# Optimization experiments

Hardware: AMD Instinct MI355X
Metric: run time of the kernel (lower is better)

Reference implementation:

```python
import jax, jax.numpy as jnp
import numpy as np
from math import sqrt

SCALE = sqrt(512.0)  # max(key_size, attn_hidden_size, query_size) with scaled=True

def setup_inputs() -> dict:
    key = jax.random.key(0)
    k1, k2, k3, k4, k5 = jax.random.split(key, 5)
    B, T, S, M, N, H = 8, 512, 512, 512, 512, 128
    return {
        "query": jax.random.normal(k1, (B, T, M), dtype=jnp.float32),
        "keys": jax.random.normal(k2, (B, S, N), dtype=jnp.float32),
        "W1": jax.random.normal(k3, (N, H), dtype=jnp.float32),
        "W2": jax.random.normal(k4, (M, H), dtype=jnp.float32),
        "v": jax.random.normal(k5, (H,), dtype=jnp.float32),
    }

def reference(query, keys, W1, W2, v):
    # Project query and keys into attention hidden space
    x1 = jnp.einsum('btm,mh->bth', query, W2)   # (B,T,H)
    x2 = jnp.einsum('bsn,nh->bsh', keys, W1)    # (B,S,H)
    # Broadcast merge (op='add'), tanh activation, v-weighted reduction over H
    merged = jnp.tanh(x1[:, :, None, :] + x2[:, None, :, :])  # (B,T,S,H)
    score = jnp.einsum('btsh,h->bts', merged, v)
    return score / SCALE
```

## Files before the change

kernel.cpp:

```cpp
#include <hip/hip_runtime.h>
#include <hip/hip_fp16.h>


constexpr float SCALE_IN  = 2.8853900817779268f;
constexpr float INV_SCALE = 0.04419417382415922f;

__global__ __launch_bounds__(512) void proj_partial_kernel(
    const float* __restrict__ q,  const float* __restrict__ w2,
    const float* __restrict__ ky, const float* __restrict__ w1,
    float* __restrict__ part) {
  __shared__ float As[64 * 64];
  __shared__ float Ws[64 * 128];

  const int khalf = blockIdx.x >> 7;
  const int rem   = blockIdx.x & 127;
  const int mat   = rem >> 6;
  const int rbase = (rem & 63) * 64;
  const float* A = mat ? ky : q;
  const float* W = mat ? w1 : w2;
  const int tid = threadIdx.x;

  const int rq = tid >> 5;
  const int hq = tid & 31;

  float acc[4][4];
#pragma unroll
  for (int r = 0; r < 4; ++r)
#pragma unroll
    for (int c = 0; c < 4; ++c) acc[r][c] = 0.0f;

  const int arow = tid >> 3;
  const int ag   = (tid & 7) * 4;
  const int wrow = tid >> 5;
  const int wg   = (tid & 31) * 4;

  const int k0 = khalf * 256;
  for (int kb = k0; kb < k0 + 256; kb += 64) {
    {
      const float* Ag = A + (size_t)(rbase + arow) * 512 + kb;
      *(float4*)(As + arow * 64 + ag)      = *(const float4*)(Ag + ag);
      *(float4*)(As + arow * 64 + ag + 32) = *(const float4*)(Ag + ag + 32);
#pragma unroll
      for (int p = 0; p < 4; ++p)
        *(float4*)(Ws + (wrow + 16 * p) * 128 + wg) =
            *(const float4*)(W + (size_t)(kb + wrow + 16 * p) * 128 + wg);
    }
    __syncthreads();
#pragma unroll 2
    for (int k4 = 0; k4 < 64; k4 += 4) {
      float a[4][4], w[4][4];
#pragma unroll
      for (int r = 0; r < 4; ++r)
        *(float4*)a[r] = *(const float4*)(As + (4 * rq + r) * 64 + k4);
#pragma unroll
      for (int kk = 0; kk < 4; ++kk)
        *(float4*)w[kk] = *(const float4*)(Ws + (k4 + kk) * 128 + 4 * hq);
#pragma unroll
      for (int kk = 0; kk < 4; ++kk)
#pragma unroll
        for (int r = 0; r < 4; ++r)
#pragma unroll
          for (int c = 0; c < 4; ++c)
            acc[r][c] = fmaf(a[r][kk], w[kk][c], acc[r][c]);
    }
    __syncthreads();
  }

  float* O = part + (size_t)(mat * 2 + khalf) * (4096 * 128);
#pragma unroll
  for (int r = 0; r < 4; ++r)
    *(float4*)(O + (size_t)(rbase + 4 * rq + r) * 128 + 4 * hq) =
        *(float4*)acc[r];
}

__global__ __launch_bounds__(256) void pack_kernel(
    const float4* __restrict__ part, uint4* __restrict__ o1,
    uint4* __restrict__ o2) {
  const int t = blockIdx.x * 256 + threadIdx.x;
  const int m = t >> 17;
  const int e = t & 131071;
  const float4 p0 = part[(size_t)(m * 2 + 0) * 131072 + e];
  const float4 p1 = part[(size_t)(m * 2 + 1) * 131072 + e];
  const float x[4] = {p0.x + p1.x, p0.y + p1.y, p0.z + p1.z, p0.w + p1.w};
  unsigned int pk[4];
#pragma unroll
  for (int c = 0; c < 4; ++c) {
    const float z  = x[c] * SCALE_IN;
    const float kf = rintf(z);
    const int   ki = (int)kf;
    const float em = __builtin_amdgcn_exp2f(z - kf);
    pk[c] = ((unsigned int)ki << 16) |
            (unsigned int)__half_as_ushort(__float2half_rn(em));
  }
  (m == 0 ? o1 : o2)[e] = *(const uint4*)pk;
}

__global__ __launch_bounds__(512, 8) void score_kernel(
    const unsigned int* __restrict__ x1w, const unsigned int* __restrict__ x2w,
    const float* __restrict__ v, float* __restrict__ out) {
  __shared__ unsigned int x1l[64 * 64];
  __shared__ unsigned int x2l[64 * 32];

  const int tid   = threadIdx.x;
  const int b     = blockIdx.x >> 7;
  const int tile  = blockIdx.x & 127;
  const int tbase = (tile >> 4) * 64;
  const int sbase = (tile & 15) * 32;

  const uint4* x1g = (const uint4*)(x1w) + (size_t)(b * 512 + tbase) * 32;
  const uint4* x2g = (const uint4*)(x2w) + (size_t)(b * 512 + sbase) * 32;

  const int sg = tid & 15;
  const int tg = tid >> 4;

  float racc[2][2] = {{0.0f, 0.0f}, {0.0f, 0.0f}};
  float sv = 0.0f;

  for (int ph = 0; ph < 2; ++ph) {
    {
      const int t1 = tid & 63;
      const int c1 = tid >> 6;
#pragma unroll
      for (int p = 0; p < 2; ++p) {
        const int c4 = c1 + 8 * p;
        const uint4 a = x1g[t1 * 32 + ph * 16 + c4];
        x1l[(4 * c4 + 0) * 64 + t1] = a.x;
        x1l[(4 * c4 + 1) * 64 + t1] = a.y;
        x1l[(4 * c4 + 2) * 64 + t1] = a.z;
        x1l[(4 * c4 + 3) * 64 + t1] = a.w;
      }
      const int s1 = tid & 31;
      const int c2 = tid >> 5;
      const uint4 c = x2g[s1 * 32 + ph * 16 + c2];
      x2l[(4 * c2 + 0) * 32 + s1] = c.x;
      x2l[(4 * c2 + 1) * 32 + s1] = c.y;
      x2l[(4 * c2 + 2) * 32 + s1] = c.z;
      x2l[(4 * c2 + 3) * 32 + s1] = c.w;
    }
    __syncthreads();

    for (int hg = 0; hg < 16; ++hg) {
      const int h0 = hg * 4;
      const float4 vq = *(const float4*)(v + ph * 64 + h0);
      sv += (vq.x + vq.y) + (vq.z + vq.w);

      float emt[2][4]; int kt[2][4];
      float ems[2][4]; int ks[2][4];
#pragma unroll
      for (int qq = 0; qq < 4; ++qq) {
        const uint2 tp = *(const uint2*)(x1l + (h0 + qq) * 64 + 2 * tg);
        emt[0][qq] = __half2float(__ushort_as_half((unsigned short)tp.x));
        kt [0][qq] = ((int)tp.x) >> 16;
        emt[1][qq] = __half2float(__ushort_as_half((unsigned short)tp.y));
        kt [1][qq] = ((int)tp.y) >> 16;
        const uint2 sp = *(const uint2*)(x2l + (h0 + qq) * 32 + 2 * sg);
        ems[0][qq] = __half2float(__ushort_as_half((unsigned short)sp.x));
        ks [0][qq] = ((int)sp.x) >> 16;
        ems[1][qq] = __half2float(__ushort_as_half((unsigned short)sp.y));
        ks [1][qq] = ((int)sp.y) >> 16;
      }

#pragma unroll
      for (int i = 0; i < 2; ++i) {
#pragma unroll
        for (int j = 0; j < 2; ++j) {
          float e[4];
#pragma unroll
          for (int qq = 0; qq < 4; ++qq) {
            int kk = kt[i][qq] + ks[j][qq];
            kk = min(kk, 30);
            e[qq] = ldexpf(emt[i][qq] * ems[j][qq], kk);
          }
          const float a0 = e[0] + 1.0f, a1 = e[1] + 1.0f;
          const float a2 = e[2] + 1.0f, a3 = e[3] + 1.0f;
          const float p12 = a0 * a1, p34 = a2 * a3;
          float u1 = vq.x * a1; u1 = fmaf(vq.y, a0, u1);
          float u2 = vq.z * a3; u2 = fmaf(vq.w, a2, u2);
          float num = u1 * p34; num = fmaf(u2, p12, num);
          const float den = p12 * p34;
          racc[i][j] = fmaf(num, __builtin_amdgcn_rcpf(den), racc[i][j]);
        }
      }
    }
    __syncthreads();
  }

  const float c1v = sv * INV_SCALE;
  const float c2v = -2.0f * INV_SCALE;
#pragma unroll
  for (int i = 0; i < 2; ++i) {
    const int t = tbase + 2 * tg + i;
    float2 o;
    o.x = fmaf(racc[i][0], c2v, c1v);
    o.y = fmaf(racc[i][1], c2v, c1v);
    *(float2*)(out + (size_t)(b * 512 + t) * 512 + sbase + 2 * sg) = o;
  }
}

extern "C" void kernel_launch(void* const* d_in, const int* in_sizes, int n_in,
                              void* d_out, int out_size, void* d_ws, size_t ws_size,
                              hipStream_t stream) {
  const float* query = (const float*)d_in[0];
  const float* keys  = (const float*)d_in[1];
  const float* W1    = (const float*)d_in[2];
  const float* W2    = (const float*)d_in[3];
  const float* v     = (const float*)d_in[4];
  float* out = (float*)d_out;

  unsigned int* x1w = (unsigned int*)d_ws;
  unsigned int* x2w = x1w + 8 * 512 * 128;

  float* part = (float*)d_out;

  hipLaunchKernelGGL(proj_partial_kernel, dim3(256), dim3(512), 0, stream,
                     query, W2, keys, W1, part);
  hipLaunchKernelGGL(pack_kernel, dim3(1024), dim3(256), 0, stream,
                     (const float4*)part, (uint4*)x1w, (uint4*)x2w);
  hipLaunchKernelGGL(score_kernel, dim3(1024), dim3(512), 0, stream,
                     x1w, x2w, v, out);
}
```

Baseline: 147.6 us.

## Replace packed exponent/mantissa factoring with direct exp2 and enlarge score tile

The pack step now only sums the split-K partials and scales them, storing plain floats instead of a packed integer exponent plus fp16 mantissa. The score kernel computes exp2 of the summed scaled projections directly, removing the half unpack, the multiply and the ldexp per element. It also doubles the S tile to 64 and gives each thread a 2x4 output block for more register reuse. The cost is one transcendental exp2 per (t,s,h) element, plus more shared memory and lower occupancy.

```diff
diff --git a/kernel.cpp b/kernel.cpp
--- a/kernel.cpp
+++ b/kernel.cpp
@@ -73,69 +73,67 @@
         *(float4*)acc[r];
 }
 
-__global__ __launch_bounds__(256) void pack_kernel(
-    const float4* __restrict__ part, uint4* __restrict__ o1,
-    uint4* __restrict__ o2) {
+__global__ __launch_bounds__(256) void combine_kernel(
+    const float4* __restrict__ part, float4* __restrict__ z1,
+    float4* __restrict__ z2) {
   const int t = blockIdx.x * 256 + threadIdx.x;
   const int m = t >> 17;
   const int e = t & 131071;
   const float4 p0 = part[(size_t)(m * 2 + 0) * 131072 + e];
   const float4 p1 = part[(size_t)(m * 2 + 1) * 131072 + e];
-  const float x[4] = {p0.x + p1.x, p0.y + p1.y, p0.z + p1.z, p0.w + p1.w};
-  unsigned int pk[4];
-#pragma unroll
-  for (int c = 0; c < 4; ++c) {
-    const float z  = x[c] * SCALE_IN;
-    const float kf = rintf(z);
-    const int   ki = (int)kf;
-    const float em = __builtin_amdgcn_exp2f(z - kf);
-    pk[c] = ((unsigned int)ki << 16) |
-            (unsigned int)__half_as_ushort(__float2half_rn(em));
-  }
-  (m == 0 ? o1 : o2)[e] = *(const uint4*)pk;
-}
-
-__global__ __launch_bounds__(512, 8) void score_kernel(
-    const unsigned int* __restrict__ x1w, const unsigned int* __restrict__ x2w,
+  float4 z;
+  z.x = (p0.x + p1.x) * SCALE_IN;
+  z.y = (p0.y + p1.y) * SCALE_IN;
+  z.z = (p0.z + p1.z) * SCALE_IN;
+  z.w = (p0.w + p1.w) * SCALE_IN;
+  (m == 0 ? z1 : z2)[e] = z;
+}
+
+__global__ __launch_bounds__(512, 4) void score_kernel(
+    const float* __restrict__ x1z, const float* __restrict__ x2z,
     const float* __restrict__ v, float* __restrict__ out) {
-  __shared__ unsigned int x1l[64 * 64];
-  __shared__ unsigned int x2l[64 * 32];
+  __shared__ float x1l[64 * 64];
+  __shared__ float x2l[64 * 64];
 
   const int tid   = threadIdx.x;
-  const int b     = blockIdx.x >> 7;
-  const int tile  = blockIdx.x & 127;
-  const int tbase = (tile >> 4) * 64;
-  const int sbase = (tile & 15) * 32;
-
-  const uint4* x1g = (const uint4*)(x1w) + (size_t)(b * 512 + tbase) * 32;
-  const uint4* x2g = (const uint4*)(x2w) + (size_t)(b * 512 + sbase) * 32;
+  const int b     = blockIdx.x >> 6;
+  const int tile  = blockIdx.x & 63;
+  const int tbase = (tile >> 3) * 64;
+  const int sbase = (tile & 7) * 64;
+
+  const float* x1g = x1z + (size_t)(b * 512 + tbase) * 128;
+  const float* x2g = x2z + (size_t)(b * 512 + sbase) * 128;
 
   const int sg = tid & 15;
   const int tg = tid >> 4;
 
-  float racc[2][2] = {{0.0f, 0.0f}, {0.0f, 0.0f}};
+  float racc[2][4];
+#pragma unroll
+  for (int i = 0; i < 2; ++i)
+#pragma unroll
+    for (int j = 0; j < 4; ++j) racc[i][j] = 0.0f;
   float sv = 0.0f;
 
   for (int ph = 0; ph < 2; ++ph) {
     {
-      const int t1 = tid & 63;
-      const int c1 = tid >> 6;
+      const int r1 = tid & 63;
+      const int c0 = tid >> 6;
 #pragma unroll
       for (int p = 0; p < 2; ++p) {
-        const int c4 = c1 + 8 * p;
-        const uint4 a = x1g[t1 * 32 + ph * 16 + c4];
-        x1l[(4 * c4 + 0) * 64 + t1] = a.x;
-        x1l[(4 * c4 + 1) * 64 + t1] = a.y;
-        x1l[(4 * c4 + 2) * 64 + t1] = a.z;
-        x1l[(4 * c4 + 3) * 64 + t1] = a.w;
+        const int c = c0 + 8 * p;
+        const float4 a =
+            *(const float4*)(x1g + (size_t)r1 * 128 + ph * 64 + 4 * c);
+        x1l[(4 * c + 0) * 64 + r1] = a.x;
+        x1l[(4 * c + 1) * 64 + r1] = a.y;
+        x1l[(4 * c + 2) * 64 + r1] = a.z;
+        x1l[(4 * c + 3) * 64 + r1] = a.w;
+        const float4 s =
+            *(const float4*)(x2g + (size_t)r1 * 128 + ph * 64 + 4 * c);
+        x2l[(4 * c + 0) * 64 + r1] = s.x;
+        x2l[(4 * c + 1) * 64 + r1] = s.y;
+        x2l[(4 * c + 2) * 64 + r1] = s.z;
+        x2l[(4 * c + 3) * 64 + r1] = s.w;
       }
-      const int s1 = tid & 31;
-      const int c2 = tid >> 5;
-      const uint4 c = x2g[s1 * 32 + ph * 16 + c2];
-      x2l[(4 * c2 + 0) * 32 + s1] = c.x;
-      x2l[(4 * c2 + 1) * 32 + s1] = c.y;
-      x2l[(4 * c2 + 2) * 32 + s1] = c.z;
-      x2l[(4 * c2 + 3) * 32 + s1] = c.w;
     }
     __syncthreads();
 
@@ -144,32 +142,29 @@
       const float4 vq = *(const float4*)(v + ph * 64 + h0);
       sv += (vq.x + vq.y) + (vq.z + vq.w);
 
-      float emt[2][4]; int kt[2][4];
-      float ems[2][4]; int ks[2][4];
+      float zt[2][4];
+      float zs[4][4];
 #pragma unroll
       for (int qq = 0; qq < 4; ++qq) {
-        const uint2 tp = *(const uint2*)(x1l + (h0 + qq) * 64 + 2 * tg);
-        emt[0][qq] = __half2float(__ushort_as_half((unsigned short)tp.x));
-        kt [0][qq] = ((int)tp.x) >> 16;
-        emt[1][qq] = __half2float(__ushort_as_half((unsigned short)tp.y));
-        kt [1][qq] = ((int)tp.y) >> 16;
-        const uint2 sp = *(const uint2*)(x2l + (h0 + qq) * 32 + 2 * sg);
-        ems[0][qq] = __half2float(__ushort_as_half((unsigned short)sp.x));
-        ks [0][qq] = ((int)sp.x) >> 16;
-        ems[1][qq] = __half2float(__ushort_as_half((unsigned short)sp.y));
-        ks [1][qq] = ((int)sp.y) >> 16;
+        const float2 tp = *(const float2*)(x1l + (h0 + qq) * 64 + 2 * tg);
+        zt[0][qq] = tp.x;
+        zt[1][qq] = tp.y;
+        const float4 sp = *(const float4*)(x2l + (h0 + qq) * 64 + 4 * sg);
+        zs[0][qq] = sp.x;
+        zs[1][qq] = sp.y;
+        zs[2][qq] = sp.z;
+        zs[3][qq] = sp.w;
       }
 
 #pragma unroll
       for (int i = 0; i < 2; ++i) {
 #pragma unroll
-        for (int j = 0; j < 2; ++j) {
+        for (int j = 0; j < 4; ++j) {
           float e[4];
 #pragma unroll
           for (int qq = 0; qq < 4; ++qq) {
-            int kk = kt[i][qq] + ks[j][qq];
-            kk = min(kk, 30);
-            e[qq] = ldexpf(emt[i][qq] * ems[j][qq], kk);
+            const float z = fminf(zt[i][qq] + zs[j][qq], 30.0f);
+            e[qq] = __builtin_amdgcn_exp2f(z);
           }
           const float a0 = e[0] + 1.0f, a1 = e[1] + 1.0f;
           const float a2 = e[2] + 1.0f, a3 = e[3] + 1.0f;
@@ -190,10 +185,12 @@
 #pragma unroll
   for (int i = 0; i < 2; ++i) {
     const int t = tbase + 2 * tg + i;
-    float2 o;
+    float4 o;
     o.x = fmaf(racc[i][0], c2v, c1v);
     o.y = fmaf(racc[i][1], c2v, c1v);
-    *(float2*)(out + (size_t)(b * 512 + t) * 512 + sbase + 2 * sg) = o;
+    o.z = fmaf(racc[i][2], c2v, c1v);
+    o.w = fmaf(racc[i][3], c2v, c1v);
+    *(float4*)(out + (size_t)(b * 512 + t) * 512 + sbase + 4 * sg) = o;
   }
 }
 
@@ -207,15 +204,15 @@
   const float* v     = (const float*)d_in[4];
   float* out = (float*)d_out;
 
-  unsigned int* x1w = (unsigned int*)d_ws;
-  unsigned int* x2w = x1w + 8 * 512 * 128;
+  float* x1zp = (float*)d_ws;
+  float* x2zp = x1zp + 8 * 512 * 128;
 
   float* part = (float*)d_out;
 
   hipLaunchKernelGGL(proj_partial_kernel, dim3(256), dim3(512), 0, stream,
                      query, W2, keys, W1, part);
-  hipLaunchKernelGGL(pack_kernel, dim3(1024), dim3(256), 0, stream,
-                     (const float4*)part, (uint4*)x1w, (uint4*)x2w);
-  hipLaunchKernelGGL(score_kernel, dim3(1024), dim3(512), 0, stream,
-                     x1w, x2w, v, out);
-}
+  hipLaunchKernelGGL(combine_kernel, dim3(1024), dim3(256), 0, stream,
+                     (const float4*)part, (float4*)x1zp, (float4*)x2zp);
+  hipLaunchKernelGGL(score_kernel, dim3(512), dim3(512), 0, stream,
+                     x1zp, x2zp, v, out);
+}
```

Measured after the change: 145.3 us. About the same (-1.5%).
